# Performance work log

Measured on AMD Instinct MI355X. Metric: run time of the kernel, lower is better.

The kernel has to match this reference:

```python
import jax, jax.numpy as jnp
import numpy as np

N_NODES = 50000
N_EDGES = 800000
N_GRAPHS = 64
IN_DIM = 108
HID = 128
OUT_DIM = 64


def setup_inputs() -> dict:
    key = jax.random.key(0)
    ks = jax.random.split(key, 10)
    x = jax.random.normal(ks[0], (N_NODES, IN_DIM - 1), dtype=jnp.float32)
    votes = jax.random.normal(ks[1], (N_NODES, 1), dtype=jnp.float32)
    edge_index = jax.random.randint(ks[2], (2, N_EDGES), 0, N_NODES, dtype=jnp.int64)
    batch = jnp.sort(jax.random.randint(ks[3], (N_NODES,), 0, N_GRAPHS, dtype=jnp.int64))
    # SAGEConv params (PyG defaults: mean aggr; lin_l has bias, lin_r has no bias)
    s1 = 1.0 / np.sqrt(IN_DIM)
    s2 = 1.0 / np.sqrt(HID)
    W1l = jax.random.uniform(ks[4], (IN_DIM, HID), jnp.float32, -s1, s1)
    b1 = jnp.zeros((HID,), jnp.float32)
    W1r = jax.random.uniform(ks[5], (IN_DIM, HID), jnp.float32, -s1, s1)
    W2l = jax.random.uniform(ks[6], (HID, OUT_DIM), jnp.float32, -s2, s2)
    b2 = jnp.zeros((OUT_DIM,), jnp.float32)
    W2r = jax.random.uniform(ks[7], (HID, OUT_DIM), jnp.float32, -s2, s2)
    return {"x": x, "votes": votes, "edge_index": edge_index, "batch": batch,
            "W1l": W1l, "b1": b1, "W1r": W1r, "W2l": W2l, "b2": b2, "W2r": W2r}


def _sage_conv(h, src, dst, Wl, b, Wr):
    # mean-aggregate neighbor features x_j at target i, then lin_l(agg) + lin_r(x_i)
    agg = jax.ops.segment_sum(h[src], dst, num_segments=h.shape[0])  # [N, d]
    deg = jax.ops.segment_sum(jnp.ones((src.shape[0],), h.dtype), dst,
                              num_segments=h.shape[0])
    agg = agg / jnp.maximum(deg, 1.0)[:, None]
    return agg @ Wl + b + h @ Wr


def reference(x, votes, edge_index, batch, W1l, b1, W1r, W2l, b2, W2r):
    src, dst = edge_index[0], edge_index[1]
    h = jnp.concatenate([x, votes], axis=1)              # [N, 108]
    h = jax.nn.relu(_sage_conv(h, src, dst, W1l, b1, W1r))  # [N, 128]
    h = _sage_conv(h, src, dst, W2l, b2, W2r)               # [N, 64]
    return jax.ops.segment_max(h, batch, num_segments=N_GRAPHS)  # [G, 64]
```

## Files before the change

### kernel.cpp

```cpp
#include <hip/hip_runtime.h>
#include <hip/hip_bf16.h>

#define IN_F 108
#define XD   107
#define HID  128
#define OUTD 64
#define SEG_NODES 64
#define BSH 6
#define BNODES 64
#define MAXBK 1024
#define EPB 4096
#define SRCMASK 0x03FFFFFF
#define BP1_N (8 * 7 * 64 * 8)
#define BP2_N (8 * 4 * 64 * 8)

typedef unsigned short ushort_t;
typedef unsigned int uint_t;
typedef __attribute__((ext_vector_type(8))) short bf16x8;
typedef __attribute__((ext_vector_type(4))) float f32x4;

__device__ inline void atomicMaxF(float* addr, float val) {
    if (val >= 0.f) atomicMax((int*)addr, __float_as_int(val));
    else            atomicMin((unsigned int*)addr, __float_as_uint(val));
}

__device__ inline ushort_t f2bf(float f) {
    uint_t b = __float_as_uint(f);
    return (ushort_t)((b + 0x7fffu + ((b >> 16) & 1u)) >> 16);
}

__global__ void init_out_kernel(float* out, int n) {
    int i = blockIdx.x * 256 + threadIdx.x;
    if (i < n) out[i] = -__builtin_inff();
}

__global__ void zero_kernel(int* p, int n) {
    int i = blockIdx.x * 256 + threadIdx.x;
    if (i < n) p[i] = 0;
}

__global__ __launch_bounds__(256) void bhist_kernel(const int* __restrict__ dst,
                                                    int* __restrict__ bcnt, int E, int nbk) {
    __shared__ int lh[MAXBK];
    for (int i = threadIdx.x; i < nbk; i += 256) lh[i] = 0;
    __syncthreads();
    int base = blockIdx.x * EPB;
    int end = min(base + EPB, E);
    for (int k = base + threadIdx.x; k < end; k += 256)
        atomicAdd(&lh[dst[k] >> BSH], 1);
    __syncthreads();
    for (int i = threadIdx.x; i < nbk; i += 256)
        if (lh[i] > 0) atomicAdd(&bcnt[i], lh[i]);
}

__global__ __launch_bounds__(64) void bscan_kernel(const int* __restrict__ bcnt,
                                                   int* __restrict__ bbase,
                                                   int* __restrict__ brsv,
                                                   int* __restrict__ row_start,
                                                   int nbk, int N, int E) {
    int lane = threadIdx.x;
    int carry = 0;
    for (int b = 0; b < nbk; b += 64) {
        int i = b + lane;
        int orig = (i < nbk) ? bcnt[i] : 0;
        int v = orig;
#pragma unroll
        for (int d = 1; d < 64; d <<= 1) {
            int t = __shfl_up(v, d);
            if (lane >= d) v += t;
        }
        if (i < nbk) {
            int ex = carry + v - orig;
            bbase[i] = ex;
            brsv[i] = ex;
        }
        carry += __shfl(v, 63);
    }
    if (lane == 0) {
        bbase[nbk] = E;
        row_start[N] = E;
    }
}

__global__ __launch_bounds__(256) void bscatter_kernel(const int* __restrict__ src,
                                                       const int* __restrict__ dst,
                                                       int* __restrict__ brsv,
                                                       uint_t* __restrict__ ebuf,
                                                       int E, int nbk) {
    __shared__ int lh[MAXBK];
    __shared__ int lofs[MAXBK];
    for (int i = threadIdx.x; i < nbk; i += 256) lh[i] = 0;
    __syncthreads();
    int base = blockIdx.x * EPB;
    int end = min(base + EPB, E);
    for (int k = base + threadIdx.x; k < end; k += 256)
        atomicAdd(&lh[dst[k] >> BSH], 1);
    __syncthreads();
    for (int i = threadIdx.x; i < nbk; i += 256)
        if (lh[i] > 0) lofs[i] = atomicAdd(&brsv[i], lh[i]);
    __syncthreads();
    for (int k = base + threadIdx.x; k < end; k += 256) {
        int d = dst[k];
        int pos = atomicAdd(&lofs[d >> BSH], 1);
        ebuf[pos] = (uint_t)src[k] | ((uint_t)(d & (BNODES - 1)) << 26);
    }
}

__global__ __launch_bounds__(256) void bbuild_kernel(const uint_t* __restrict__ ebuf,
                                                     const int* __restrict__ bbase,
                                                     int* __restrict__ row_start,
                                                     int* __restrict__ sorted_src,
                                                     int N) {
    __shared__ int nh[BNODES];
    __shared__ int cur[BNODES];
    int b = blockIdx.x;
    int e0 = bbase[b], e1 = bbase[b + 1];
    int nlo = b << BSH;
    int nloc = min(BNODES, N - nlo);
    if (threadIdx.x < BNODES) nh[threadIdx.x] = 0;
    __syncthreads();
    for (int k = e0 + threadIdx.x; k < e1; k += 256)
        atomicAdd(&nh[ebuf[k] >> 26], 1);
    __syncthreads();
    if (threadIdx.x < 64) {
        int lane = threadIdx.x;
        int orig = nh[lane];
        int v = orig;
#pragma unroll
        for (int d = 1; d < 64; d <<= 1) {
            int t = __shfl_up(v, d);
            if (lane >= d) v += t;
        }
        int ex = e0 + v - orig;
        cur[lane] = ex;
        if (lane < nloc) row_start[nlo + lane] = ex;
    }
    __syncthreads();
    for (int k = e0 + threadIdx.x; k < e1; k += 256) {
        uint_t e = ebuf[k];
        int pos = atomicAdd(&cur[e >> 26], 1);
        sorted_src[pos] = (int)(e & SRCMASK);
    }
}

__global__ void convert_kernel(const float* __restrict__ x, const float* __restrict__ votes,
                               ushort_t* __restrict__ xb, int N) {
    int idx = blockIdx.x * 256 + threadIdx.x;
    if (idx >= N * IN_F) return;
    int n = idx / IN_F, f = idx - n * IN_F;
    float v = (f < XD) ? x[n * XD + f] : votes[n];
    xb[idx] = f2bf(v);
}

__global__ void convertw_kernel(const float* __restrict__ W1l, const float* __restrict__ W1r,
                                const float* __restrict__ W2l, const float* __restrict__ W2r,
                                ushort_t* __restrict__ bp1, ushort_t* __restrict__ bp2) {
    int i = blockIdx.x * 256 + threadIdx.x;
    if (i < BP1_N) {
        int j = i & 7;
        int lane = (i >> 3) & 63;
        int rest = i >> 9;
        int ks = rest % 7;
        int ct = rest / 7;
        int k = ks * 32 + (lane >> 4) * 8 + j;
        int col = ct * 16 + (lane & 15);
        float v = 0.f;
        if (k < IN_F) v = W1l[k * HID + col];
        else if (k < 2 * IN_F) v = W1r[(k - IN_F) * HID + col];
        bp1[i] = f2bf(v);
    }
    int i2 = i - BP1_N;
    if (i2 >= 0 && i2 < BP2_N) {
        int j = i2 & 7;
        int lane = (i2 >> 3) & 63;
        int ks = (i2 >> 9) & 3;
        int ct = i2 >> 11;
        int k = ks * 32 + (lane >> 4) * 8 + j;
        int col = ct * 16 + (lane & 15);
        float v = (col < OUTD) ? W2l[k * OUTD + col] : W2r[k * OUTD + (col - OUTD)];
        bp2[i2] = f2bf(v);
    }
}

__global__ __launch_bounds__(256) void gather1_kernel(
        const ushort_t* __restrict__ xb,
        const int* __restrict__ row_start, const int* __restrict__ sorted_src,
        ushort_t* __restrict__ agg1b, int N) {
    int node = (blockIdx.x * 256 + threadIdx.x) >> 6;
    int lane = threadIdx.x & 63;
    if (node >= N) return;
    int rs = row_start[node], re = row_start[node + 1];
    int h  = lane >> 5;
    int l2 = lane & 31;
    float a0 = 0.f, a1 = 0.f, a2 = 0.f, a3 = 0.f;
    for (int k0 = rs; k0 < re; k0 += 64) {
        int cnt = min(64, re - k0);
        int sl = sorted_src[k0 + min(lane, cnt - 1)];
        int t = 0;
        for (; t + 8 <= cnt; t += 8) {
            int s0 = __shfl(sl, t + h);
            int s1 = __shfl(sl, t + 2 + h);
            int s2 = __shfl(sl, t + 4 + h);
            int s3 = __shfl(sl, t + 6 + h);
            if (l2 < 27) {
                uint2 w0 = *(const uint2*)(xb + s0 * IN_F + 4 * l2);
                uint2 w1 = *(const uint2*)(xb + s1 * IN_F + 4 * l2);
                uint2 w2 = *(const uint2*)(xb + s2 * IN_F + 4 * l2);
                uint2 w3 = *(const uint2*)(xb + s3 * IN_F + 4 * l2);
                a0 += __uint_as_float(w0.x << 16) + __uint_as_float(w1.x << 16)
                    + __uint_as_float(w2.x << 16) + __uint_as_float(w3.x << 16);
                a1 += __uint_as_float(w0.x & 0xffff0000u) + __uint_as_float(w1.x & 0xffff0000u)
                    + __uint_as_float(w2.x & 0xffff0000u) + __uint_as_float(w3.x & 0xffff0000u);
                a2 += __uint_as_float(w0.y << 16) + __uint_as_float(w1.y << 16)
                    + __uint_as_float(w2.y << 16) + __uint_as_float(w3.y << 16);
                a3 += __uint_as_float(w0.y & 0xffff0000u) + __uint_as_float(w1.y & 0xffff0000u)
                    + __uint_as_float(w2.y & 0xffff0000u) + __uint_as_float(w3.y & 0xffff0000u);
            }
        }
        for (; t < cnt; t += 2) {
            int tt = min(t + h, cnt - 1);
            int s = __shfl(sl, tt);
            if (t + h < cnt && l2 < 27) {
                uint2 w = *(const uint2*)(xb + s * IN_F + 4 * l2);
                a0 += __uint_as_float(w.x << 16);
                a1 += __uint_as_float(w.x & 0xffff0000u);
                a2 += __uint_as_float(w.y << 16);
                a3 += __uint_as_float(w.y & 0xffff0000u);
            }
        }
    }
    a0 += __shfl_xor(a0, 32);
    a1 += __shfl_xor(a1, 32);
    a2 += __shfl_xor(a2, 32);
    a3 += __shfl_xor(a3, 32);
    float inv = 1.f / fmaxf((float)(re - rs), 1.f);
    if (lane < 27) {
        ushort4 p;
        p.x = f2bf(a0 * inv);
        p.y = f2bf(a1 * inv);
        p.z = f2bf(a2 * inv);
        p.w = f2bf(a3 * inv);
        *(ushort4*)(agg1b + node * IN_F + 4 * lane) = p;
    }
}

__global__ __launch_bounds__(256) void gatheru_kernel(
        const ushort_t* __restrict__ ub,
        const int* __restrict__ row_start, const int* __restrict__ sorted_src,
        float* __restrict__ aggu, int N) {
    int node = (blockIdx.x * 256 + threadIdx.x) >> 6;
    int lane = threadIdx.x & 63;
    if (node >= N) return;
    int rs = row_start[node], re = row_start[node + 1];
    int g  = lane >> 4;
    int l4 = lane & 15;
    float a0 = 0.f, a1 = 0.f, a2 = 0.f, a3 = 0.f;
    for (int k0 = rs; k0 < re; k0 += 64) {
        int cnt = min(64, re - k0);
        int sl = sorted_src[k0 + min(lane, cnt - 1)];
        int t = 0;
        for (; t + 8 <= cnt; t += 8) {
            int s0 = __shfl(sl, t + g);
            int s1 = __shfl(sl, t + 4 + g);
            uint2 w0 = *(const uint2*)(ub + (s0 << 6) + 4 * l4);
            uint2 w1 = *(const uint2*)(ub + (s1 << 6) + 4 * l4);
            a0 += __uint_as_float(w0.x << 16) + __uint_as_float(w1.x << 16);
            a1 += __uint_as_float(w0.x & 0xffff0000u) + __uint_as_float(w1.x & 0xffff0000u);
            a2 += __uint_as_float(w0.y << 16) + __uint_as_float(w1.y << 16);
            a3 += __uint_as_float(w0.y & 0xffff0000u) + __uint_as_float(w1.y & 0xffff0000u);
        }
        for (; t < cnt; t += 4) {
            int tt = min(t + g, cnt - 1);
            int s = __shfl(sl, tt);
            if (t + g < cnt) {
                uint2 w = *(const uint2*)(ub + (s << 6) + 4 * l4);
                a0 += __uint_as_float(w.x << 16);
                a1 += __uint_as_float(w.x & 0xffff0000u);
                a2 += __uint_as_float(w.y << 16);
                a3 += __uint_as_float(w.y & 0xffff0000u);
            }
        }
    }
    a0 += __shfl_xor(a0, 16); a0 += __shfl_xor(a0, 32);
    a1 += __shfl_xor(a1, 16); a1 += __shfl_xor(a1, 32);
    a2 += __shfl_xor(a2, 16); a2 += __shfl_xor(a2, 32);
    a3 += __shfl_xor(a3, 16); a3 += __shfl_xor(a3, 32);
    float inv = 1.f / fmaxf((float)(re - rs), 1.f);
    if (lane < 16) {
        *(float4*)(aggu + (node << 6) + 4 * lane) =
            make_float4(a0 * inv, a1 * inv, a2 * inv, a3 * inv);
    }
}

#define T1_M 32
#define A_STRIDE_US 232
#define A_STRIDE_U  116
#define H1_STRIDE_US 136
__global__ __launch_bounds__(256) void gemm1_kernel(
        const ushort_t* __restrict__ xb, const ushort_t* __restrict__ agg1b,
        const ushort_t* __restrict__ bp1, const ushort_t* __restrict__ bp2,
        const float* __restrict__ b1,
        ushort_t* __restrict__ ub, float* __restrict__ vv, int N) {
    __shared__ uint_t smem[T1_M * A_STRIDE_U];
    int n0 = blockIdx.x * T1_M;
    for (int i = threadIdx.x; i < T1_M * 112; i += 256) {
        int m = i / 112, c = i - m * 112;
        int n = n0 + m;
        uint_t v = 0u;
        if (n < N) {
            if (c < 54)       v = ((const uint_t*)(agg1b + n * IN_F))[c];
            else if (c < 108) v = ((const uint_t*)(xb + n * IN_F))[c - 54];
        }
        smem[m * A_STRIDE_U + c] = v;
    }
    __syncthreads();

    int lane = threadIdx.x & 63;
    int wid  = threadIdx.x >> 6;
    int wrow = (wid & 1) << 4;
    int wcol = (wid >> 1) << 6;
    int arow = wrow + (lane & 15);
    int akoff = (lane >> 4) * 8;
    const ushort_t* sA = (const ushort_t*)smem;
    const bf16x8* bp1v = (const bf16x8*)bp1;

    f32x4 acc0 = {}, acc1 = {}, acc2_ = {}, acc3 = {};
    int ct0 = wcol >> 4;
#pragma unroll
    for (int ks = 0; ks < 7; ++ks) {
        bf16x8 af = *(const bf16x8*)(sA + arow * A_STRIDE_US + ks * 32 + akoff);
        bf16x8 bf0 = bp1v[((ct0 + 0) * 7 + ks) * 64 + lane];
        bf16x8 bf1 = bp1v[((ct0 + 1) * 7 + ks) * 64 + lane];
        bf16x8 bf2 = bp1v[((ct0 + 2) * 7 + ks) * 64 + lane];
        bf16x8 bf3 = bp1v[((ct0 + 3) * 7 + ks) * 64 + lane];
        acc0 = __builtin_amdgcn_mfma_f32_16x16x32_bf16(af, bf0, acc0, 0, 0, 0);
        acc1 = __builtin_amdgcn_mfma_f32_16x16x32_bf16(af, bf1, acc1, 0, 0, 0);
        acc2_ = __builtin_amdgcn_mfma_f32_16x16x32_bf16(af, bf2, acc2_, 0, 0, 0);
        acc3 = __builtin_amdgcn_mfma_f32_16x16x32_bf16(af, bf3, acc3, 0, 0, 0);
    }

    __syncthreads();
    ushort_t* sh1 = (ushort_t*)smem;
    {
        int colb = wcol + (lane & 15);
        int rowb = wrow + ((lane >> 4) << 2);
#pragma unroll
        for (int t = 0; t < 4; ++t) {
            f32x4 a = (t == 0) ? acc0 : (t == 1) ? acc1 : (t == 2) ? acc2_ : acc3;
            int col = colb + t * 16;
            float bj = b1[col];
#pragma unroll
            for (int r = 0; r < 4; ++r)
                sh1[(rowb + r) * H1_STRIDE_US + col] = f2bf(fmaxf(a[r] + bj, 0.f));
        }
    }
    __syncthreads();

    const bf16x8* bp2v = (const bf16x8*)bp2;
    f32x4 dcc0 = {}, dcc1 = {}, dcc2 = {}, dcc3 = {};
#pragma unroll
    for (int ks = 0; ks < 4; ++ks) {
        bf16x8 af = *(const bf16x8*)(sh1 + arow * H1_STRIDE_US + ks * 32 + akoff);
        bf16x8 bf0 = bp2v[((ct0 + 0) * 4 + ks) * 64 + lane];
        bf16x8 bf1 = bp2v[((ct0 + 1) * 4 + ks) * 64 + lane];
        bf16x8 bf2 = bp2v[((ct0 + 2) * 4 + ks) * 64 + lane];
        bf16x8 bf3 = bp2v[((ct0 + 3) * 4 + ks) * 64 + lane];
        dcc0 = __builtin_amdgcn_mfma_f32_16x16x32_bf16(af, bf0, dcc0, 0, 0, 0);
        dcc1 = __builtin_amdgcn_mfma_f32_16x16x32_bf16(af, bf1, dcc1, 0, 0, 0);
        dcc2 = __builtin_amdgcn_mfma_f32_16x16x32_bf16(af, bf2, dcc2, 0, 0, 0);
        dcc3 = __builtin_amdgcn_mfma_f32_16x16x32_bf16(af, bf3, dcc3, 0, 0, 0);
    }

    {
        int colb = wcol + (lane & 15);
        int rowb = wrow + ((lane >> 4) << 2);
#pragma unroll
        for (int t = 0; t < 4; ++t) {
            f32x4 a = (t == 0) ? dcc0 : (t == 1) ? dcc1 : (t == 2) ? dcc2 : dcc3;
            int col = colb + t * 16;
#pragma unroll
            for (int r = 0; r < 4; ++r) {
                int n = n0 + rowb + r;
                if (n < N) {
                    if (col < OUTD) ub[(n << 6) + col] = f2bf(a[r]);
                    else            vv[(n << 6) + (col - OUTD)] = a[r];
                }
            }
        }
    }
}

__global__ __launch_bounds__(256) void finalize_kernel(
        const float* __restrict__ aggu, const float* __restrict__ vv,
        const float* __restrict__ b2, const int* __restrict__ batch,
        float* __restrict__ out, int N) {
    int j  = threadIdx.x & 63;
    int nq = threadIdx.x >> 6;
    int n0 = blockIdx.x * SEG_NODES;
    float bj = b2[j];
    int curg = -1;
    float curm = -__builtin_inff();
    for (int m = nq; m < SEG_NODES; m += 4) {
        int n = n0 + m;
        if (n >= N) break;
        int g = batch[n];
        float v = aggu[(n << 6) + j] + vv[(n << 6) + j] + bj;
        if (g != curg) {
            if (curg >= 0) atomicMaxF(&out[(curg << 6) + j], curm);
            curg = g;
            curm = v;
        } else {
            curm = fmaxf(curm, v);
        }
    }
    if (curg >= 0) atomicMaxF(&out[(curg << 6) + j], curm);
}

static inline size_t align256(size_t v) { return (v + 255) & ~(size_t)255; }

extern "C" void kernel_launch(void* const* d_in, const int* in_sizes, int n_in,
                              void* d_out, int out_size, void* d_ws, size_t ws_size,
                              hipStream_t stream) {
    const float* x     = (const float*)d_in[0];
    const float* votes = (const float*)d_in[1];
    const int*   eidx  = (const int*)d_in[2];
    const int*   batch = (const int*)d_in[3];
    const float* W1l   = (const float*)d_in[4];
    const float* b1    = (const float*)d_in[5];
    const float* W1r   = (const float*)d_in[6];
    const float* W2l   = (const float*)d_in[7];
    const float* b2    = (const float*)d_in[8];
    const float* W2r   = (const float*)d_in[9];
    float* out = (float*)d_out;

    const int N = in_sizes[1];
    const int E = in_sizes[2] / 2;
    const int* src = eidx;
    const int* dst = eidx + E;
    const int nbk = (N + BNODES - 1) >> BSH;

    char* ws = (char*)d_ws;
    size_t off = 0;
    int* bcnt       = (int*)(ws + off); off = align256(off + (size_t)nbk * 4);
    int* bbase      = (int*)(ws + off); off = align256(off + (size_t)(nbk + 1) * 4);
    int* brsv       = (int*)(ws + off); off = align256(off + (size_t)nbk * 4);
    int* row_start  = (int*)(ws + off); off = align256(off + (size_t)(N + 1) * 4);
    uint_t* ebuf    = (uint_t*)(ws + off); off = align256(off + (size_t)E * 4);
    int* sorted_src = (int*)(ws + off); off = align256(off + (size_t)E * 4);
    ushort_t* xb    = (ushort_t*)(ws + off); off = align256(off + (size_t)N * IN_F * 2);
    ushort_t* agg1b = (ushort_t*)(ws + off); off = align256(off + (size_t)N * IN_F * 2);
    ushort_t* ub    = (ushort_t*)(ws + off); off = align256(off + (size_t)N * OUTD * 2);
    float* vv       = (float*)(ws + off); off = align256(off + (size_t)N * OUTD * 4);
    float* aggu     = (float*)(ws + off); off = align256(off + (size_t)N * OUTD * 4);
    ushort_t* bp1   = (ushort_t*)(ws + off); off = align256(off + (size_t)BP1_N * 2);
    ushort_t* bp2   = (ushort_t*)(ws + off); off = align256(off + (size_t)BP2_N * 2);

    zero_kernel<<<(nbk + 255) / 256, 256, 0, stream>>>(bcnt, nbk);
    init_out_kernel<<<(out_size + 255) / 256, 256, 0, stream>>>(out, out_size);

    int nebl = (E + EPB - 1) / EPB;
    bhist_kernel<<<nebl, 256, 0, stream>>>(dst, bcnt, E, nbk);
    bscan_kernel<<<1, 64, 0, stream>>>(bcnt, bbase, brsv, row_start, nbk, N, E);
    bscatter_kernel<<<nebl, 256, 0, stream>>>(src, dst, brsv, ebuf, E, nbk);
    bbuild_kernel<<<nbk, 256, 0, stream>>>(ebuf, bbase, row_start, sorted_src, N);

    convert_kernel<<<(N * IN_F + 255) / 256, 256, 0, stream>>>(x, votes, xb, N);
    convertw_kernel<<<(BP1_N + BP2_N + 255) / 256, 256, 0, stream>>>(W1l, W1r, W2l, W2r,
                                                                     bp1, bp2);

    gather1_kernel<<<(N + 3) / 4, 256, 0, stream>>>(xb, row_start, sorted_src, agg1b, N);
    gemm1_kernel<<<(N + T1_M - 1) / T1_M, 256, 0, stream>>>(xb, agg1b, bp1, bp2,
                                                            b1, ub, vv, N);
    gatheru_kernel<<<(N + 3) / 4, 256, 0, stream>>>(ub, row_start, sorted_src, aggu, N);

    finalize_kernel<<<(N + SEG_NODES - 1) / SEG_NODES, 256, 0, stream>>>(
        aggu, vv, b2, batch, out, N);
}
```

Before: 148.0 us.

## Fuse layer-1 neighbor gather into the MFMA GEMM kernel and merge prep launches

Layer-1 mean aggregation now runs inside the GEMM kernel, writing averaged neighbor rows straight into shared memory instead of round-tripping through a global agg1b buffer. Each block of 4 waves gathers 32 nodes (8 per wave) before the MFMA stages. The two zeroing/init kernels and the two conversion kernels are also merged to cut launch count. The trade-off is less parallelism during the gather phase, since only 4 waves per 32 nodes do latency-bound gathers, and the GEMM waits behind the slowest gather in the block.

After: 132.8 us. -10.3%, faster.

```diff
diff --git a/kernel.cpp b/kernel.cpp
--- a/kernel.cpp
+++ b/kernel.cpp
@@ -29,14 +29,10 @@
     return (ushort_t)((b + 0x7fffu + ((b >> 16) & 1u)) >> 16);
 }
 
-__global__ void init_out_kernel(float* out, int n) {
+__global__ void init0_kernel(int* bcnt, int nbk, float* out, int n) {
     int i = blockIdx.x * 256 + threadIdx.x;
+    if (i < nbk) bcnt[i] = 0;
     if (i < n) out[i] = -__builtin_inff();
-}
-
-__global__ void zero_kernel(int* p, int n) {
-    int i = blockIdx.x * 256 + threadIdx.x;
-    if (i < n) p[i] = 0;
 }
 
 __global__ __launch_bounds__(256) void bhist_kernel(const int* __restrict__ dst,
@@ -143,23 +139,21 @@
     }
 }
 
-__global__ void convert_kernel(const float* __restrict__ x, const float* __restrict__ votes,
-                               ushort_t* __restrict__ xb, int N) {
+__global__ void prep_kernel(const float* __restrict__ x, const float* __restrict__ votes,
+                            const float* __restrict__ W1l, const float* __restrict__ W1r,
+                            const float* __restrict__ W2l, const float* __restrict__ W2r,
+                            ushort_t* __restrict__ xb, ushort_t* __restrict__ bp1,
+                            ushort_t* __restrict__ bp2, int N) {
     int idx = blockIdx.x * 256 + threadIdx.x;
-    if (idx >= N * IN_F) return;
-    int n = idx / IN_F, f = idx - n * IN_F;
-    float v = (f < XD) ? x[n * XD + f] : votes[n];
-    xb[idx] = f2bf(v);
-}
-
-__global__ void convertw_kernel(const float* __restrict__ W1l, const float* __restrict__ W1r,
-                                const float* __restrict__ W2l, const float* __restrict__ W2r,
-                                ushort_t* __restrict__ bp1, ushort_t* __restrict__ bp2) {
-    int i = blockIdx.x * 256 + threadIdx.x;
-    if (i < BP1_N) {
-        int j = i & 7;
-        int lane = (i >> 3) & 63;
-        int rest = i >> 9;
+    if (idx < N * IN_F) {
+        int n = idx / IN_F, f = idx - n * IN_F;
+        float v = (f < XD) ? x[n * XD + f] : votes[n];
+        xb[idx] = f2bf(v);
+    }
+    if (idx < BP1_N) {
+        int j = idx & 7;
+        int lane = (idx >> 3) & 63;
+        int rest = idx >> 9;
         int ks = rest % 7;
         int ct = rest / 7;
         int k = ks * 32 + (lane >> 4) * 8 + j;
@@ -167,9 +161,9 @@
         float v = 0.f;
         if (k < IN_F) v = W1l[k * HID + col];
         else if (k < 2 * IN_F) v = W1r[(k - IN_F) * HID + col];
-        bp1[i] = f2bf(v);
-    }
-    int i2 = i - BP1_N;
+        bp1[idx] = f2bf(v);
+    }
+    int i2 = idx - BP1_N;
     if (i2 >= 0 && i2 < BP2_N) {
         int j = i2 & 7;
         int lane = (i2 >> 3) & 63;
@@ -182,65 +176,166 @@
     }
 }
 
-__global__ __launch_bounds__(256) void gather1_kernel(
+#define T1_M 32
+#define A_STRIDE_US 232
+#define A_STRIDE_U  116
+#define H1_STRIDE_US 136
+__global__ __launch_bounds__(256) void fused1_kernel(
         const ushort_t* __restrict__ xb,
         const int* __restrict__ row_start, const int* __restrict__ sorted_src,
-        ushort_t* __restrict__ agg1b, int N) {
-    int node = (blockIdx.x * 256 + threadIdx.x) >> 6;
+        const ushort_t* __restrict__ bp1, const ushort_t* __restrict__ bp2,
+        const float* __restrict__ b1,
+        ushort_t* __restrict__ ub, float* __restrict__ vv, int N) {
+    __shared__ uint_t smem[T1_M * A_STRIDE_U];
+    int n0 = blockIdx.x * T1_M;
+    const uint_t* xbu = (const uint_t*)xb;
+
+    for (int i = threadIdx.x; i < T1_M * 54; i += 256) {
+        int m = i / 54, c = i - m * 54;
+        int n = n0 + m;
+        smem[m * A_STRIDE_U + 54 + c] = (n < N) ? xbu[n * 54 + c] : 0u;
+    }
+    for (int i = threadIdx.x; i < T1_M * 4; i += 256) {
+        int m = i >> 2, c = i & 3;
+        smem[m * A_STRIDE_U + 108 + c] = 0u;
+    }
+
     int lane = threadIdx.x & 63;
-    if (node >= N) return;
-    int rs = row_start[node], re = row_start[node + 1];
+    int wid  = threadIdx.x >> 6;
     int h  = lane >> 5;
     int l2 = lane & 31;
-    float a0 = 0.f, a1 = 0.f, a2 = 0.f, a3 = 0.f;
-    for (int k0 = rs; k0 < re; k0 += 64) {
-        int cnt = min(64, re - k0);
-        int sl = sorted_src[k0 + min(lane, cnt - 1)];
-        int t = 0;
-        for (; t + 8 <= cnt; t += 8) {
-            int s0 = __shfl(sl, t + h);
-            int s1 = __shfl(sl, t + 2 + h);
-            int s2 = __shfl(sl, t + 4 + h);
-            int s3 = __shfl(sl, t + 6 + h);
-            if (l2 < 27) {
-                uint2 w0 = *(const uint2*)(xb + s0 * IN_F + 4 * l2);
-                uint2 w1 = *(const uint2*)(xb + s1 * IN_F + 4 * l2);
-                uint2 w2 = *(const uint2*)(xb + s2 * IN_F + 4 * l2);
-                uint2 w3 = *(const uint2*)(xb + s3 * IN_F + 4 * l2);
-                a0 += __uint_as_float(w0.x << 16) + __uint_as_float(w1.x << 16)
-                    + __uint_as_float(w2.x << 16) + __uint_as_float(w3.x << 16);
-                a1 += __uint_as_float(w0.x & 0xffff0000u) + __uint_as_float(w1.x & 0xffff0000u)
-                    + __uint_as_float(w2.x & 0xffff0000u) + __uint_as_float(w3.x & 0xffff0000u);
-                a2 += __uint_as_float(w0.y << 16) + __uint_as_float(w1.y << 16)
-                    + __uint_as_float(w2.y << 16) + __uint_as_float(w3.y << 16);
-                a3 += __uint_as_float(w0.y & 0xffff0000u) + __uint_as_float(w1.y & 0xffff0000u)
-                    + __uint_as_float(w2.y & 0xffff0000u) + __uint_as_float(w3.y & 0xffff0000u);
+
+    for (int it = 0; it < 8; ++it) {
+        int m = wid * 8 + it;
+        int node = n0 + m;
+        float a0 = 0.f, a1 = 0.f, a2 = 0.f, a3 = 0.f;
+        int deg = 0;
+        if (node < N) {
+            int rs = row_start[node], re = row_start[node + 1];
+            deg = re - rs;
+            for (int k0 = rs; k0 < re; k0 += 64) {
+                int cnt = min(64, re - k0);
+                int sl = sorted_src[k0 + min(lane, cnt - 1)];
+                int t = 0;
+                for (; t + 8 <= cnt; t += 8) {
+                    int s0 = __shfl(sl, t + h);
+                    int s1 = __shfl(sl, t + 2 + h);
+                    int s2 = __shfl(sl, t + 4 + h);
+                    int s3 = __shfl(sl, t + 6 + h);
+                    if (l2 < 27) {
+                        uint2 w0 = *(const uint2*)(xb + s0 * IN_F + 4 * l2);
+                        uint2 w1 = *(const uint2*)(xb + s1 * IN_F + 4 * l2);
+                        uint2 w2 = *(const uint2*)(xb + s2 * IN_F + 4 * l2);
+                        uint2 w3 = *(const uint2*)(xb + s3 * IN_F + 4 * l2);
+                        a0 += __uint_as_float(w0.x << 16) + __uint_as_float(w1.x << 16)
+                            + __uint_as_float(w2.x << 16) + __uint_as_float(w3.x << 16);
+                        a1 += __uint_as_float(w0.x & 0xffff0000u) + __uint_as_float(w1.x & 0xffff0000u)
+                            + __uint_as_float(w2.x & 0xffff0000u) + __uint_as_float(w3.x & 0xffff0000u);
+                        a2 += __uint_as_float(w0.y << 16) + __uint_as_float(w1.y << 16)
+                            + __uint_as_float(w2.y << 16) + __uint_as_float(w3.y << 16);
+                        a3 += __uint_as_float(w0.y & 0xffff0000u) + __uint_as_float(w1.y & 0xffff0000u)
+                            + __uint_as_float(w2.y & 0xffff0000u) + __uint_as_float(w3.y & 0xffff0000u);
+                    }
+                }
+                for (; t < cnt; t += 2) {
+                    int tt = min(t + h, cnt - 1);
+                    int s = __shfl(sl, tt);
+                    if (t + h < cnt && l2 < 27) {
+                        uint2 w = *(const uint2*)(xb + s * IN_F + 4 * l2);
+                        a0 += __uint_as_float(w.x << 16);
+                        a1 += __uint_as_float(w.x & 0xffff0000u);
+                        a2 += __uint_as_float(w.y << 16);
+                        a3 += __uint_as_float(w.y & 0xffff0000u);
+                    }
+                }
             }
         }
-        for (; t < cnt; t += 2) {
-            int tt = min(t + h, cnt - 1);
-            int s = __shfl(sl, tt);
-            if (t + h < cnt && l2 < 27) {
-                uint2 w = *(const uint2*)(xb + s * IN_F + 4 * l2);
-                a0 += __uint_as_float(w.x << 16);
-                a1 += __uint_as_float(w.x & 0xffff0000u);
-                a2 += __uint_as_float(w.y << 16);
-                a3 += __uint_as_float(w.y & 0xffff0000u);
+        a0 += __shfl_xor(a0, 32);
+        a1 += __shfl_xor(a1, 32);
+        a2 += __shfl_xor(a2, 32);
+        a3 += __shfl_xor(a3, 32);
+        if (node < N && l2 < 27) {
+            float inv = 1.f / fmaxf((float)deg, 1.f);
+            ushort4 p;
+            p.x = f2bf(a0 * inv);
+            p.y = f2bf(a1 * inv);
+            p.z = f2bf(a2 * inv);
+            p.w = f2bf(a3 * inv);
+            *(ushort4*)((ushort_t*)smem + m * A_STRIDE_US + 4 * l2) = p;
+        }
+    }
+    __syncthreads();
+
+    int wrow = (wid & 1) << 4;
+    int wcol = (wid >> 1) << 6;
+    int arow = wrow + (lane & 15);
+    int akoff = (lane >> 4) * 8;
+    const ushort_t* sA = (const ushort_t*)smem;
+    const bf16x8* bp1v = (const bf16x8*)bp1;
+
+    f32x4 acc0 = {}, acc1 = {}, acc2_ = {}, acc3 = {};
+    int ct0 = wcol >> 4;
+#pragma unroll
+    for (int ks = 0; ks < 7; ++ks) {
+        bf16x8 af = *(const bf16x8*)(sA + arow * A_STRIDE_US + ks * 32 + akoff);
+        bf16x8 bf0 = bp1v[((ct0 + 0) * 7 + ks) * 64 + lane];
+        bf16x8 bf1 = bp1v[((ct0 + 1) * 7 + ks) * 64 + lane];
+        bf16x8 bf2 = bp1v[((ct0 + 2) * 7 + ks) * 64 + lane];
+        bf16x8 bf3 = bp1v[((ct0 + 3) * 7 + ks) * 64 + lane];
+        acc0 = __builtin_amdgcn_mfma_f32_16x16x32_bf16(af, bf0, acc0, 0, 0, 0);
+        acc1 = __builtin_amdgcn_mfma_f32_16x16x32_bf16(af, bf1, acc1, 0, 0, 0);
+        acc2_ = __builtin_amdgcn_mfma_f32_16x16x32_bf16(af, bf2, acc2_, 0, 0, 0);
+        acc3 = __builtin_amdgcn_mfma_f32_16x16x32_bf16(af, bf3, acc3, 0, 0, 0);
+    }
+
+    __syncthreads();
+    ushort_t* sh1 = (ushort_t*)smem;
+    {
+        int colb = wcol + (lane & 15);
+        int rowb = wrow + ((lane >> 4) << 2);
+#pragma unroll
+        for (int t = 0; t < 4; ++t) {
+            f32x4 a = (t == 0) ? acc0 : (t == 1) ? acc1 : (t == 2) ? acc2_ : acc3;
+            int col = colb + t * 16;
+            float bj = b1[col];
+#pragma unroll
+            for (int r = 0; r < 4; ++r)
+                sh1[(rowb + r) * H1_STRIDE_US + col] = f2bf(fmaxf(a[r] + bj, 0.f));
+        }
+    }
+    __syncthreads();
+
+    const bf16x8* bp2v = (const bf16x8*)bp2;
+    f32x4 dcc0 = {}, dcc1 = {}, dcc2 = {}, dcc3 = {};
+#pragma unroll
+    for (int ks = 0; ks < 4; ++ks) {
+        bf16x8 af = *(const bf16x8*)(sh1 + arow * H1_STRIDE_US + ks * 32 + akoff);
+        bf16x8 bf0 = bp2v[((ct0 + 0) * 4 + ks) * 64 + lane];
+        bf16x8 bf1 = bp2v[((ct0 + 1) * 4 + ks) * 64 + lane];
+        bf16x8 bf2 = bp2v[((ct0 + 2) * 4 + ks) * 64 + lane];
+        bf16x8 bf3 = bp2v[((ct0 + 3) * 4 + ks) * 64 + lane];
+        dcc0 = __builtin_amdgcn_mfma_f32_16x16x32_bf16(af, bf0, dcc0, 0, 0, 0);
+        dcc1 = __builtin_amdgcn_mfma_f32_16x16x32_bf16(af, bf1, dcc1, 0, 0, 0);
+        dcc2 = __builtin_amdgcn_mfma_f32_16x16x32_bf16(af, bf2, dcc2, 0, 0, 0);
+        dcc3 = __builtin_amdgcn_mfma_f32_16x16x32_bf16(af, bf3, dcc3, 0, 0, 0);
+    }
+
+    {
+        int colb = wcol + (lane & 15);
+        int rowb = wrow + ((lane >> 4) << 2);
+#pragma unroll
+        for (int t = 0; t < 4; ++t) {
+            f32x4 a = (t == 0) ? dcc0 : (t == 1) ? dcc1 : (t == 2) ? dcc2 : dcc3;
+            int col = colb + t * 16;
+#pragma unroll
+            for (int r = 0; r < 4; ++r) {
+                int n = n0 + rowb + r;
+                if (n < N) {
+                    if (col < OUTD) ub[(n << 6) + col] = f2bf(a[r]);
+                    else            vv[(n << 6) + (col - OUTD)] = a[r];
+                }
             }
         }
-    }
-    a0 += __shfl_xor(a0, 32);
-    a1 += __shfl_xor(a1, 32);
-    a2 += __shfl_xor(a2, 32);
-    a3 += __shfl_xor(a3, 32);
-    float inv = 1.f / fmaxf((float)(re - rs), 1.f);
-    if (lane < 27) {
-        ushort4 p;
-        p.x = f2bf(a0 * inv);
-        p.y = f2bf(a1 * inv);
-        p.z = f2bf(a2 * inv);
-        p.w = f2bf(a3 * inv);
-        *(ushort4*)(agg1b + node * IN_F + 4 * lane) = p;
     }
 }
 
@@ -292,104 +387,6 @@
     }
 }
 
-#define T1_M 32
-#define A_STRIDE_US 232
-#define A_STRIDE_U  116
-#define H1_STRIDE_US 136
-__global__ __launch_bounds__(256) void gemm1_kernel(
-        const ushort_t* __restrict__ xb, const ushort_t* __restrict__ agg1b,
-        const ushort_t* __restrict__ bp1, const ushort_t* __restrict__ bp2,
-        const float* __restrict__ b1,
-        ushort_t* __restrict__ ub, float* __restrict__ vv, int N) {
-    __shared__ uint_t smem[T1_M * A_STRIDE_U];
-    int n0 = blockIdx.x * T1_M;
-    for (int i = threadIdx.x; i < T1_M * 112; i += 256) {
-        int m = i / 112, c = i - m * 112;
-        int n = n0 + m;
-        uint_t v = 0u;
-        if (n < N) {
-            if (c < 54)       v = ((const uint_t*)(agg1b + n * IN_F))[c];
-            else if (c < 108) v = ((const uint_t*)(xb + n * IN_F))[c - 54];
-        }
-        smem[m * A_STRIDE_U + c] = v;
-    }
-    __syncthreads();
-
-    int lane = threadIdx.x & 63;
-    int wid  = threadIdx.x >> 6;
-    int wrow = (wid & 1) << 4;
-    int wcol = (wid >> 1) << 6;
-    int arow = wrow + (lane & 15);
-    int akoff = (lane >> 4) * 8;
-    const ushort_t* sA = (const ushort_t*)smem;
-    const bf16x8* bp1v = (const bf16x8*)bp1;
-
-    f32x4 acc0 = {}, acc1 = {}, acc2_ = {}, acc3 = {};
-    int ct0 = wcol >> 4;
-#pragma unroll
-    for (int ks = 0; ks < 7; ++ks) {
-        bf16x8 af = *(const bf16x8*)(sA + arow * A_STRIDE_US + ks * 32 + akoff);
-        bf16x8 bf0 = bp1v[((ct0 + 0) * 7 + ks) * 64 + lane];
-        bf16x8 bf1 = bp1v[((ct0 + 1) * 7 + ks) * 64 + lane];
-        bf16x8 bf2 = bp1v[((ct0 + 2) * 7 + ks) * 64 + lane];
-        bf16x8 bf3 = bp1v[((ct0 + 3) * 7 + ks) * 64 + lane];
-        acc0 = __builtin_amdgcn_mfma_f32_16x16x32_bf16(af, bf0, acc0, 0, 0, 0);
-        acc1 = __builtin_amdgcn_mfma_f32_16x16x32_bf16(af, bf1, acc1, 0, 0, 0);
-        acc2_ = __builtin_amdgcn_mfma_f32_16x16x32_bf16(af, bf2, acc2_, 0, 0, 0);
-        acc3 = __builtin_amdgcn_mfma_f32_16x16x32_bf16(af, bf3, acc3, 0, 0, 0);
-    }
-
-    __syncthreads();
-    ushort_t* sh1 = (ushort_t*)smem;
-    {
-        int colb = wcol + (lane & 15);
-        int rowb = wrow + ((lane >> 4) << 2);
-#pragma unroll
-        for (int t = 0; t < 4; ++t) {
-            f32x4 a = (t == 0) ? acc0 : (t == 1) ? acc1 : (t == 2) ? acc2_ : acc3;
-            int col = colb + t * 16;
-            float bj = b1[col];
-#pragma unroll
-            for (int r = 0; r < 4; ++r)
-                sh1[(rowb + r) * H1_STRIDE_US + col] = f2bf(fmaxf(a[r] + bj, 0.f));
-        }
-    }
-    __syncthreads();
-
-    const bf16x8* bp2v = (const bf16x8*)bp2;
-    f32x4 dcc0 = {}, dcc1 = {}, dcc2 = {}, dcc3 = {};
-#pragma unroll
-    for (int ks = 0; ks < 4; ++ks) {
-        bf16x8 af = *(const bf16x8*)(sh1 + arow * H1_STRIDE_US + ks * 32 + akoff);
-        bf16x8 bf0 = bp2v[((ct0 + 0) * 4 + ks) * 64 + lane];
-        bf16x8 bf1 = bp2v[((ct0 + 1) * 4 + ks) * 64 + lane];
-        bf16x8 bf2 = bp2v[((ct0 + 2) * 4 + ks) * 64 + lane];
-        bf16x8 bf3 = bp2v[((ct0 + 3) * 4 + ks) * 64 + lane];
-        dcc0 = __builtin_amdgcn_mfma_f32_16x16x32_bf16(af, bf0, dcc0, 0, 0, 0);
-        dcc1 = __builtin_amdgcn_mfma_f32_16x16x32_bf16(af, bf1, dcc1, 0, 0, 0);
-        dcc2 = __builtin_amdgcn_mfma_f32_16x16x32_bf16(af, bf2, dcc2, 0, 0, 0);
-        dcc3 = __builtin_amdgcn_mfma_f32_16x16x32_bf16(af, bf3, dcc3, 0, 0, 0);
-    }
-
-    {
-        int colb = wcol + (lane & 15);
-        int rowb = wrow + ((lane >> 4) << 2);
-#pragma unroll
-        for (int t = 0; t < 4; ++t) {
-            f32x4 a = (t == 0) ? dcc0 : (t == 1) ? dcc1 : (t == 2) ? dcc2 : dcc3;
-            int col = colb + t * 16;
-#pragma unroll
-            for (int r = 0; r < 4; ++r) {
-                int n = n0 + rowb + r;
-                if (n < N) {
-                    if (col < OUTD) ub[(n << 6) + col] = f2bf(a[r]);
-                    else            vv[(n << 6) + (col - OUTD)] = a[r];
-                }
-            }
-        }
-    }
-}
-
 __global__ __launch_bounds__(256) void finalize_kernel(
         const float* __restrict__ aggu, const float* __restrict__ vv,
         const float* __restrict__ b2, const int* __restrict__ batch,
@@ -448,15 +445,16 @@
     uint_t* ebuf    = (uint_t*)(ws + off); off = align256(off + (size_t)E * 4);
     int* sorted_src = (int*)(ws + off); off = align256(off + (size_t)E * 4);
     ushort_t* xb    = (ushort_t*)(ws + off); off = align256(off + (size_t)N * IN_F * 2);
-    ushort_t* agg1b = (ushort_t*)(ws + off); off = align256(off + (size_t)N * IN_F * 2);
     ushort_t* ub    = (ushort_t*)(ws + off); off = align256(off + (size_t)N * OUTD * 2);
     float* vv       = (float*)(ws + off); off = align256(off + (size_t)N * OUTD * 4);
     float* aggu     = (float*)(ws + off); off = align256(off + (size_t)N * OUTD * 4);
     ushort_t* bp1   = (ushort_t*)(ws + off); off = align256(off + (size_t)BP1_N * 2);
     ushort_t* bp2   = (ushort_t*)(ws + off); off = align256(off + (size_t)BP2_N * 2);
 
-    zero_kernel<<<(nbk + 255) / 256, 256, 0, stream>>>(bcnt, nbk);
-    init_out_kernel<<<(out_size + 255) / 256, 256, 0, stream>>>(out, out_size);
+    {
+        int mx = max(nbk, out_size);
+        init0_kernel<<<(mx + 255) / 256, 256, 0, stream>>>(bcnt, nbk, out, out_size);
+    }
 
     int nebl = (E + EPB - 1) / EPB;
     bhist_kernel<<<nebl, 256, 0, stream>>>(dst, bcnt, E, nbk);
@@ -464,13 +462,11 @@
     bscatter_kernel<<<nebl, 256, 0, stream>>>(src, dst, brsv, ebuf, E, nbk);
     bbuild_kernel<<<nbk, 256, 0, stream>>>(ebuf, bbase, row_start, sorted_src, N);
 
-    convert_kernel<<<(N * IN_F + 255) / 256, 256, 0, stream>>>(x, votes, xb, N);
-    convertw_kernel<<<(BP1_N + BP2_N + 255) / 256, 256, 0, stream>>>(W1l, W1r, W2l, W2r,
-                                                                     bp1, bp2);
-
-    gather1_kernel<<<(N + 3) / 4, 256, 0, stream>>>(xb, row_start, sorted_src, agg1b, N);
-    gemm1_kernel<<<(N + T1_M - 1) / T1_M, 256, 0, stream>>>(xb, agg1b, bp1, bp2,
-                                                            b1, ub, vv, N);
+    prep_kernel<<<(N * IN_F + 255) / 256, 256, 0, stream>>>(x, votes, W1l, W1r, W2l, W2r,
+                                                            xb, bp1, bp2, N);
+
+    fused1_kernel<<<(N + T1_M - 1) / T1_M, 256, 0, stream>>>(xb, row_start, sorted_src,
+                                                             bp1, bp2, b1, ub, vv, N);
     gatheru_kernel<<<(N + 3) / 4, 256, 0, stream>>>(ub, row_start, sorted_src, aggu, N);
 
     finalize_kernel<<<(N + SEG_NODES - 1) / SEG_NODES, 256, 0, stream>>>(
```
